# Kernel optimization log

Measured on AMD Instinct MI355X. Metric: run time of the kernel, lower is better.

Reference implementation:

```python
import jax, jax.numpy as jnp
import numpy as np

N_NODES = 100000


def _sage_conv(x, edge_index, W_n, W_s, b):
    # edge_index: [2, E] with row0 = src, row1 = dst (messages flow src -> dst)
    src, dst = edge_index[0], edge_index[1]
    msgs = x[src]                                   # [E, F] gather
    summed = jax.ops.segment_sum(msgs, dst, num_segments=N_NODES)   # [N, F]
    deg = jax.ops.segment_sum(jnp.ones((edge_index.shape[1],), x.dtype), dst,
                              num_segments=N_NODES)                 # [N]
    mean = summed / jnp.maximum(deg, 1.0)[:, None]  # mean aggregation
    return mean @ W_n + x @ W_s + b


def setup_inputs() -> dict:
    key = jax.random.key(0)
    ks = jax.random.split(key, 8)
    in_dim, hid_dim, out_dim = 64, 64, 32
    n_edges = 1600000
    x = jax.random.normal(ks[0], (N_NODES, in_dim), dtype=jnp.float32)
    edge_index = jax.random.randint(ks[1], (2, n_edges), 0, N_NODES, dtype=jnp.int64)
    s1 = 1.0 / np.sqrt(in_dim)
    s2 = 1.0 / np.sqrt(hid_dim)
    W1_n = jax.random.uniform(ks[2], (in_dim, hid_dim), jnp.float32, -s1, s1)
    W1_s = jax.random.uniform(ks[3], (in_dim, hid_dim), jnp.float32, -s1, s1)
    b1 = jnp.zeros((hid_dim,), jnp.float32)
    W2_n = jax.random.uniform(ks[4], (hid_dim, out_dim), jnp.float32, -s2, s2)
    W2_s = jax.random.uniform(ks[5], (hid_dim, out_dim), jnp.float32, -s2, s2)
    b2 = jnp.zeros((out_dim,), jnp.float32)
    return {"x": x, "edge_index": edge_index, "W1_n": W1_n, "W1_s": W1_s,
            "b1": b1, "W2_n": W2_n, "W2_s": W2_s, "b2": b2}


def reference(x, edge_index, W1_n, W1_s, b1, W2_n, W2_s, b2):
    h = _sage_conv(x, edge_index, W1_n, W1_s, b1)
    h = jax.nn.relu(h)
    # dropout(p=0.5) is identity in eval mode
    out = _sage_conv(h, edge_index, W2_n, W2_s, b2)
    return out
```

## Files before the change

### kernel.cpp

```cpp
#include <hip/hip_runtime.h>
#include <hip/hip_bf16.h>

#define N_NODES 100000
#define NB 784
#define NPAD 100352
#define BSH 7
#define BMASK 127
#define CAP 4096
#define APAD 68

__device__ inline void fma4(float a, const float4& w, float4& c) {
  c.x = fmaf(a, w.x, c.x);
  c.y = fmaf(a, w.y, c.y);
  c.z = fmaf(a, w.z, c.z);
  c.w = fmaf(a, w.w, c.w);
}
__device__ inline unsigned short f2bf(float f) {
  unsigned u = __float_as_uint(f);
  u += 0x7fffu + ((u >> 16) & 1u);
  return (unsigned short)(u >> 16);
}
__device__ inline float bflo(unsigned u) { return __uint_as_float(u << 16); }
__device__ inline float bfhi(unsigned u) { return __uint_as_float(u & 0xffff0000u); }

__global__ __launch_bounds__(256) void bscatter_k(const int* __restrict__ src,
                                                  const int* __restrict__ dst,
                                                  unsigned* __restrict__ bcur,
                                                  unsigned* __restrict__ ep,
                                                  int E) {
  __shared__ unsigned lh[NB];
  __shared__ unsigned lbase[NB];
  for (int i = threadIdx.x; i < NB; i += 256) lh[i] = 0;
  __syncthreads();
  const int base = blockIdx.x * 4096;
  unsigned short rank[16];
  unsigned short bb[16];
#pragma unroll
  for (int it = 0; it < 16; ++it) {
    int e = base + it * 256 + threadIdx.x;
    if (e < E) {
      unsigned b = ((unsigned)dst[e]) >> BSH;
      bb[it] = (unsigned short)b;
      rank[it] = (unsigned short)atomicAdd(&lh[b], 1u);
    }
  }
  __syncthreads();
  for (int i = threadIdx.x; i < NB; i += 256)
    lbase[i] = lh[i] ? atomicAdd(&bcur[i], lh[i]) : 0u;
  __syncthreads();
#pragma unroll
  for (int it = 0; it < 16; ++it) {
    int e = base + it * 256 + threadIdx.x;
    if (e < E) {
      unsigned b = bb[it];
      ep[(size_t)b * CAP + lbase[b] + rank[it]] =
          (((unsigned)src[e]) << BSH) | (((unsigned)dst[e]) & BMASK);
    }
  }
}

#define GB1 1563

__global__ __launch_bounds__(256) void fused1_k(
    const float* __restrict__ x, const float* __restrict__ W1n,
    const float* __restrict__ W1s, const float* __restrict__ b1,
    unsigned short* __restrict__ xnb, float* __restrict__ xs,
    const unsigned* __restrict__ ep, const unsigned* __restrict__ bcur,
    int* __restrict__ ssrc, uint2* __restrict__ rows2, int M) {
  __shared__ __align__(16) float smem[12544];
  const int tid = threadIdx.x;

  if (blockIdx.x >= GB1) {
    const int b = blockIdx.x - GB1;
    unsigned* cnt = (unsigned*)smem;
    unsigned* sc = cnt + 128;
    const unsigned cntb = bcur[b];
    const unsigned beg = (unsigned)(b * CAP);
    if (tid < 128) cnt[tid] = 0;
    __syncthreads();
    for (unsigned j = tid; j < cntb; j += 256)
      atomicAdd(&cnt[ep[(size_t)beg + j] & BMASK], 1u);
    __syncthreads();
    unsigned v = (tid < 128) ? cnt[tid] : 0u;
    if (tid < 128) sc[tid] = v;
    __syncthreads();
    for (int off = 1; off < 128; off <<= 1) {
      unsigned t = (tid < 128 && tid >= off) ? sc[tid - off] : 0u;
      __syncthreads();
      if (tid < 128) sc[tid] += t;
      __syncthreads();
    }
    if (tid < 128) {
      unsigned ex = sc[tid] - v;
      rows2[b * 128 + tid] = make_uint2(beg + ex, beg + ex + v);
      cnt[tid] = ex;
    }
    __syncthreads();
    for (unsigned j = tid; j < cntb; j += 256) {
      unsigned p = ep[(size_t)beg + j];
      unsigned r = atomicAdd(&cnt[p & BMASK], 1u);
      ssrc[(size_t)beg + r] = (int)(p >> BSH);
    }
    return;
  }

  float* Wn = smem;
  float* Ws = smem + 4096;
  float* Ax = smem + 8192;
  const int row0 = blockIdx.x * 64;

  for (int i = tid; i < 1024; i += 256) {
    ((float4*)Wn)[i] = ((const float4*)W1n)[i];
    ((float4*)Ws)[i] = ((const float4*)W1s)[i];
  }
  for (int i = tid; i < 1024; i += 256) {
    int r = i >> 4, c = i & 15;
    long long gr = row0 + r;
    if (gr >= M) gr = M - 1;
    float4 v = ((const float4*)(x + gr * 64))[c];
    *(float4*)&Ax[r * APAD + 4 * c] = v;
  }
  __syncthreads();

  const int tx = tid & 15;
  const int ty = tid >> 4;
  const int arow = ty * 4;

  float4 an[4], as[4];
#pragma unroll
  for (int r = 0; r < 4; ++r) {
    an[r] = make_float4(0.f, 0.f, 0.f, 0.f);
    as[r] = make_float4(0.f, 0.f, 0.f, 0.f);
  }

#pragma unroll 1
  for (int k4 = 0; k4 < 16; ++k4) {
    float4 wn0 = *(const float4*)&Wn[(4 * k4 + 0) * 64 + 4 * tx];
    float4 wn1 = *(const float4*)&Wn[(4 * k4 + 1) * 64 + 4 * tx];
    float4 wn2 = *(const float4*)&Wn[(4 * k4 + 2) * 64 + 4 * tx];
    float4 wn3 = *(const float4*)&Wn[(4 * k4 + 3) * 64 + 4 * tx];
    float4 ws0 = *(const float4*)&Ws[(4 * k4 + 0) * 64 + 4 * tx];
    float4 ws1 = *(const float4*)&Ws[(4 * k4 + 1) * 64 + 4 * tx];
    float4 ws2 = *(const float4*)&Ws[(4 * k4 + 2) * 64 + 4 * tx];
    float4 ws3 = *(const float4*)&Ws[(4 * k4 + 3) * 64 + 4 * tx];
#pragma unroll
    for (int r = 0; r < 4; ++r) {
      float4 a = *(const float4*)&Ax[(arow + r) * APAD + 4 * k4];
      fma4(a.x, wn0, an[r]);
      fma4(a.y, wn1, an[r]);
      fma4(a.z, wn2, an[r]);
      fma4(a.w, wn3, an[r]);
      fma4(a.x, ws0, as[r]);
      fma4(a.y, ws1, as[r]);
      fma4(a.z, ws2, as[r]);
      fma4(a.w, ws3, as[r]);
    }
  }

  const float4 bv = *(const float4*)&b1[4 * tx];
#pragma unroll
  for (int r = 0; r < 4; ++r) {
    int row = row0 + arow + r;
    if (row < M) {
      float4 o;
      o.x = as[r].x + bv.x;
      o.y = as[r].y + bv.y;
      o.z = as[r].z + bv.z;
      o.w = as[r].w + bv.w;
      *(float4*)&xs[(long long)row * 64 + 4 * tx] = o;
      ushort4 p;
      p.x = f2bf(an[r].x);
      p.y = f2bf(an[r].y);
      p.z = f2bf(an[r].z);
      p.w = f2bf(an[r].w);
      *(ushort4*)&xnb[(long long)row * 64 + 4 * tx] = p;
    }
  }
}

__global__ __launch_bounds__(256) void gemm2_k(
    const float* __restrict__ h, const float* __restrict__ W2n,
    const float* __restrict__ W2s, const float* __restrict__ b2,
    unsigned short* __restrict__ hnb, float* __restrict__ hs, int M) {
  __shared__ float Wn[64 * 32];
  __shared__ float Ws[64 * 32];
  __shared__ float Ah[128 * APAD];
  const int tid = threadIdx.x;
  const int row0 = blockIdx.x * 128;

  for (int i = tid; i < 512; i += 256) {
    ((float4*)Wn)[i] = ((const float4*)W2n)[i];
    ((float4*)Ws)[i] = ((const float4*)W2s)[i];
  }
  for (int i = tid; i < 2048; i += 256) {
    int r = i >> 4, c = i & 15;
    long long gr = row0 + r;
    if (gr >= M) gr = M - 1;
    float4 v = ((const float4*)(h + gr * 64))[c];
    *(float4*)&Ah[r * APAD + 4 * c] = v;
  }
  __syncthreads();

  const int tx = tid & 7;
  const int ty = tid >> 3;
  const int arow = ty * 4;

  float4 an[4], as[4];
#pragma unroll
  for (int r = 0; r < 4; ++r) {
    an[r] = make_float4(0.f, 0.f, 0.f, 0.f);
    as[r] = make_float4(0.f, 0.f, 0.f, 0.f);
  }

#pragma unroll 1
  for (int k4 = 0; k4 < 16; ++k4) {
    float4 wn0 = *(const float4*)&Wn[(4 * k4 + 0) * 32 + 4 * tx];
    float4 wn1 = *(const float4*)&Wn[(4 * k4 + 1) * 32 + 4 * tx];
    float4 wn2 = *(const float4*)&Wn[(4 * k4 + 2) * 32 + 4 * tx];
    float4 wn3 = *(const float4*)&Wn[(4 * k4 + 3) * 32 + 4 * tx];
    float4 ws0 = *(const float4*)&Ws[(4 * k4 + 0) * 32 + 4 * tx];
    float4 ws1 = *(const float4*)&Ws[(4 * k4 + 1) * 32 + 4 * tx];
    float4 ws2 = *(const float4*)&Ws[(4 * k4 + 2) * 32 + 4 * tx];
    float4 ws3 = *(const float4*)&Ws[(4 * k4 + 3) * 32 + 4 * tx];
#pragma unroll
    for (int r = 0; r < 4; ++r) {
      float4 a = *(const float4*)&Ah[(arow + r) * APAD + 4 * k4];
      fma4(a.x, wn0, an[r]);
      fma4(a.y, wn1, an[r]);
      fma4(a.z, wn2, an[r]);
      fma4(a.w, wn3, an[r]);
      fma4(a.x, ws0, as[r]);
      fma4(a.y, ws1, as[r]);
      fma4(a.z, ws2, as[r]);
      fma4(a.w, ws3, as[r]);
    }
  }

  const float4 bv = *(const float4*)&b2[4 * tx];
#pragma unroll
  for (int r = 0; r < 4; ++r) {
    int row = row0 + arow + r;
    if (row < M) {
      float4 o;
      o.x = as[r].x + bv.x;
      o.y = as[r].y + bv.y;
      o.z = as[r].z + bv.z;
      o.w = as[r].w + bv.w;
      *(float4*)&hs[(long long)row * 32 + 4 * tx] = o;
      ushort4 p;
      p.x = f2bf(an[r].x);
      p.y = f2bf(an[r].y);
      p.z = f2bf(an[r].z);
      p.w = f2bf(an[r].w);
      *(ushort4*)&hnb[(long long)row * 32 + 4 * tx] = p;
    }
  }
}

template <int LOGF, bool RELU>
__global__ __launch_bounds__(256) void gatherb_k(
    const uint4* __restrict__ valb4, const int* __restrict__ ssrc,
    const uint2* __restrict__ rows2, const float* __restrict__ base,
    float* __restrict__ out, int N) {
  constexpr int P = (1 << LOGF) / 8;
  const int node = blockIdx.x * (256 / P) + threadIdx.x / P;
  const int p = threadIdx.x & (P - 1);
  if (node >= N) return;
  const uint2 be = rows2[node];
  const unsigned beg = be.x, end = be.y;

  float acc[8];
#pragma unroll
  for (int q = 0; q < 8; ++q) acc[q] = 0.f;

  unsigned j = beg;
  for (; j + 8 <= end; j += 8) {
    int sn[8];
#pragma unroll
    for (int i = 0; i < 8; ++i) sn[i] = ssrc[j + i];
    uint4 u[8];
#pragma unroll
    for (int i = 0; i < 8; ++i) u[i] = valb4[(size_t)sn[i] * P + p];
#pragma unroll
    for (int i = 0; i < 8; ++i) {
      acc[0] += bflo(u[i].x);
      acc[1] += bfhi(u[i].x);
      acc[2] += bflo(u[i].y);
      acc[3] += bfhi(u[i].y);
      acc[4] += bflo(u[i].z);
      acc[5] += bfhi(u[i].z);
      acc[6] += bflo(u[i].w);
      acc[7] += bfhi(u[i].w);
    }
  }
  if (j < end) {
    const unsigned last = end - 1;
    int sn[8];
#pragma unroll
    for (int i = 0; i < 8; ++i) {
      unsigned jj = j + i;
      sn[i] = ssrc[jj < last ? jj : last];
    }
    uint4 u[8];
#pragma unroll
    for (int i = 0; i < 8; ++i) u[i] = valb4[(size_t)sn[i] * P + p];
#pragma unroll
    for (int i = 0; i < 8; ++i) {
      bool ok = (j + i) < end;
      acc[0] += ok ? bflo(u[i].x) : 0.f;
      acc[1] += ok ? bfhi(u[i].x) : 0.f;
      acc[2] += ok ? bflo(u[i].y) : 0.f;
      acc[3] += ok ? bfhi(u[i].y) : 0.f;
      acc[4] += ok ? bflo(u[i].z) : 0.f;
      acc[5] += ok ? bfhi(u[i].z) : 0.f;
      acc[6] += ok ? bflo(u[i].w) : 0.f;
      acc[7] += ok ? bfhi(u[i].w) : 0.f;
    }
  }

  const unsigned dg = end - beg;
  const float inv = dg ? 1.f / (float)dg : 0.f;
  const size_t o = (size_t)node * (8 * P) + 8 * p;
  float4 b0 = *(const float4*)&base[o];
  float4 b1 = *(const float4*)&base[o + 4];
  float4 o0, o1;
  o0.x = acc[0] * inv + b0.x;
  o0.y = acc[1] * inv + b0.y;
  o0.z = acc[2] * inv + b0.z;
  o0.w = acc[3] * inv + b0.w;
  o1.x = acc[4] * inv + b1.x;
  o1.y = acc[5] * inv + b1.y;
  o1.z = acc[6] * inv + b1.z;
  o1.w = acc[7] * inv + b1.w;
  if (RELU) {
    o0.x = fmaxf(o0.x, 0.f);
    o0.y = fmaxf(o0.y, 0.f);
    o0.z = fmaxf(o0.z, 0.f);
    o0.w = fmaxf(o0.w, 0.f);
    o1.x = fmaxf(o1.x, 0.f);
    o1.y = fmaxf(o1.y, 0.f);
    o1.z = fmaxf(o1.z, 0.f);
    o1.w = fmaxf(o1.w, 0.f);
  }
  *(float4*)&out[o] = o0;
  *(float4*)&out[o + 4] = o1;
}

extern "C" void kernel_launch(void* const* d_in, const int* in_sizes, int n_in,
                              void* d_out, int out_size, void* d_ws,
                              size_t ws_size, hipStream_t stream) {
  const float* x   = (const float*)d_in[0];
  const int*   ei  = (const int*)d_in[1];
  const float* W1n = (const float*)d_in[2];
  const float* W1s = (const float*)d_in[3];
  const float* b1  = (const float*)d_in[4];
  const float* W2n = (const float*)d_in[5];
  const float* W2s = (const float*)d_in[6];
  const float* b2  = (const float*)d_in[7];
  float* out = (float*)d_out;

  const int E = in_sizes[1] / 2;
  const int M = N_NODES;
  const int* src = ei;
  const int* dst = ei + E;

  char* wsb = (char*)d_ws;
  unsigned*       ep    = (unsigned*)(wsb);
  int*            ssrc  = (int*)(wsb + 12845056);
  uint2*          rows2 = (uint2*)(wsb + 25690112);
  unsigned*       bcur  = (unsigned*)(wsb + 26492928);
  unsigned short* xnb   = (unsigned short*)(wsb + 26496064);
  float*          xs    = (float*)(wsb + 39296064);
  float*          h     = (float*)(wsb + 64896064);
  unsigned short* hnb   = xnb;
  float*          hs    = xs;

  hipMemsetAsync(bcur, 0, NB * 4, stream);
  bscatter_k<<<(E + 4095) / 4096, 256, 0, stream>>>(src, dst, bcur, ep, E);
  fused1_k<<<GB1 + NB, 256, 0, stream>>>(x, W1n, W1s, b1, xnb, xs, ep, bcur,
                                         ssrc, rows2, M);
  gatherb_k<6, true><<<(M + 31) / 32, 256, 0, stream>>>(
      (const uint4*)xnb, ssrc, rows2, xs, h, M);
  gemm2_k<<<(M + 127) / 128, 256, 0, stream>>>(h, W2n, W2s, b2, hnb, hs, M);
  gatherb_k<5, false><<<(M + 63) / 64, 256, 0, stream>>>(
      (const uint4*)hnb, ssrc, rows2, hs, out, M);
}
```

Baseline: 237.1 us.

## Store layer-1 mean as bf16 and fuse residual+ReLU into layer-2 GEMM load

The layer-1 gather now writes only the mean aggregation, packed as bf16. The self-term add and ReLU move into the gemm2 tile load, which reads both the bf16 mean and the fp32 self term. This halves the gather's write traffic and avoids reading the self term in the gather, but adds another bf16 rounding of the hidden activations before they reach the second layer. The bucket-scatter kernel also moves to 1024-thread blocks, each handling 16K edges, to cut global atomics. Workspace buffers are remapped so that hnb reuses the edge-pointer region and hs the former h region.

```diff
diff --git a/kernel.cpp b/kernel.cpp
--- a/kernel.cpp
+++ b/kernel.cpp
@@ -20,24 +20,30 @@
   u += 0x7fffu + ((u >> 16) & 1u);
   return (unsigned short)(u >> 16);
 }
+__device__ inline unsigned pack2bf(float a, float b) {
+  return (unsigned)f2bf(a) | ((unsigned)f2bf(b) << 16);
+}
 __device__ inline float bflo(unsigned u) { return __uint_as_float(u << 16); }
 __device__ inline float bfhi(unsigned u) { return __uint_as_float(u & 0xffff0000u); }
-
-__global__ __launch_bounds__(256) void bscatter_k(const int* __restrict__ src,
-                                                  const int* __restrict__ dst,
-                                                  unsigned* __restrict__ bcur,
-                                                  unsigned* __restrict__ ep,
-                                                  int E) {
+__device__ inline float bf2f(unsigned short u) {
+  return __uint_as_float((unsigned)u << 16);
+}
+
+__global__ __launch_bounds__(1024) void bscatter_k(const int* __restrict__ src,
+                                                   const int* __restrict__ dst,
+                                                   unsigned* __restrict__ bcur,
+                                                   unsigned* __restrict__ ep,
+                                                   int E) {
   __shared__ unsigned lh[NB];
   __shared__ unsigned lbase[NB];
-  for (int i = threadIdx.x; i < NB; i += 256) lh[i] = 0;
+  for (int i = threadIdx.x; i < NB; i += 1024) lh[i] = 0;
   __syncthreads();
-  const int base = blockIdx.x * 4096;
+  const int base = blockIdx.x * 16384;
   unsigned short rank[16];
   unsigned short bb[16];
 #pragma unroll
   for (int it = 0; it < 16; ++it) {
-    int e = base + it * 256 + threadIdx.x;
+    int e = base + it * 1024 + threadIdx.x;
     if (e < E) {
       unsigned b = ((unsigned)dst[e]) >> BSH;
       bb[it] = (unsigned short)b;
@@ -45,12 +51,12 @@
     }
   }
   __syncthreads();
-  for (int i = threadIdx.x; i < NB; i += 256)
+  for (int i = threadIdx.x; i < NB; i += 1024)
     lbase[i] = lh[i] ? atomicAdd(&bcur[i], lh[i]) : 0u;
   __syncthreads();
 #pragma unroll
   for (int it = 0; it < 16; ++it) {
-    int e = base + it * 256 + threadIdx.x;
+    int e = base + it * 1024 + threadIdx.x;
     if (e < E) {
       unsigned b = bb[it];
       ep[(size_t)b * CAP + lbase[b] + rank[it]] =
@@ -178,10 +184,80 @@
   }
 }
 
+__global__ __launch_bounds__(256) void gather1_k(
+    const uint4* __restrict__ valb4, const int* __restrict__ ssrc,
+    const uint2* __restrict__ rows2, uint4* __restrict__ meanb, int N) {
+  constexpr int P = 8;
+  const int node = blockIdx.x * (256 / P) + threadIdx.x / P;
+  const int p = threadIdx.x & (P - 1);
+  if (node >= N) return;
+  const uint2 be = rows2[node];
+  const unsigned beg = be.x, end = be.y;
+
+  float acc[8];
+#pragma unroll
+  for (int q = 0; q < 8; ++q) acc[q] = 0.f;
+
+  unsigned j = beg;
+  for (; j + 8 <= end; j += 8) {
+    int sn[8];
+#pragma unroll
+    for (int i = 0; i < 8; ++i) sn[i] = ssrc[j + i];
+    uint4 u[8];
+#pragma unroll
+    for (int i = 0; i < 8; ++i) u[i] = valb4[(size_t)sn[i] * P + p];
+#pragma unroll
+    for (int i = 0; i < 8; ++i) {
+      acc[0] += bflo(u[i].x);
+      acc[1] += bfhi(u[i].x);
+      acc[2] += bflo(u[i].y);
+      acc[3] += bfhi(u[i].y);
+      acc[4] += bflo(u[i].z);
+      acc[5] += bfhi(u[i].z);
+      acc[6] += bflo(u[i].w);
+      acc[7] += bfhi(u[i].w);
+    }
+  }
+  if (j < end) {
+    const unsigned last = end - 1;
+    int sn[8];
+#pragma unroll
+    for (int i = 0; i < 8; ++i) {
+      unsigned jj = j + i;
+      sn[i] = ssrc[jj < last ? jj : last];
+    }
+    uint4 u[8];
+#pragma unroll
+    for (int i = 0; i < 8; ++i) u[i] = valb4[(size_t)sn[i] * P + p];
+#pragma unroll
+    for (int i = 0; i < 8; ++i) {
+      bool ok = (j + i) < end;
+      acc[0] += ok ? bflo(u[i].x) : 0.f;
+      acc[1] += ok ? bfhi(u[i].x) : 0.f;
+      acc[2] += ok ? bflo(u[i].y) : 0.f;
+      acc[3] += ok ? bfhi(u[i].y) : 0.f;
+      acc[4] += ok ? bflo(u[i].z) : 0.f;
+      acc[5] += ok ? bfhi(u[i].z) : 0.f;
+      acc[6] += ok ? bflo(u[i].w) : 0.f;
+      acc[7] += ok ? bfhi(u[i].w) : 0.f;
+    }
+  }
+
+  const unsigned dg = end - beg;
+  const float inv = dg ? 1.f / (float)dg : 0.f;
+  uint4 pk;
+  pk.x = pack2bf(acc[0] * inv, acc[1] * inv);
+  pk.y = pack2bf(acc[2] * inv, acc[3] * inv);
+  pk.z = pack2bf(acc[4] * inv, acc[5] * inv);
+  pk.w = pack2bf(acc[6] * inv, acc[7] * inv);
+  meanb[(size_t)node * P + p] = pk;
+}
+
 __global__ __launch_bounds__(256) void gemm2_k(
-    const float* __restrict__ h, const float* __restrict__ W2n,
-    const float* __restrict__ W2s, const float* __restrict__ b2,
-    unsigned short* __restrict__ hnb, float* __restrict__ hs, int M) {
+    const unsigned short* __restrict__ mean1, const float* __restrict__ xs,
+    const float* __restrict__ W2n, const float* __restrict__ W2s,
+    const float* __restrict__ b2, unsigned short* __restrict__ hnb,
+    float* __restrict__ hs, int M) {
   __shared__ float Wn[64 * 32];
   __shared__ float Ws[64 * 32];
   __shared__ float Ah[128 * APAD];
@@ -196,7 +272,13 @@
     int r = i >> 4, c = i & 15;
     long long gr = row0 + r;
     if (gr >= M) gr = M - 1;
-    float4 v = ((const float4*)(h + gr * 64))[c];
+    float4 sv = ((const float4*)(xs + gr * 64))[c];
+    ushort4 mv = ((const ushort4*)(mean1 + gr * 64))[c];
+    float4 v;
+    v.x = fmaxf(bf2f(mv.x) + sv.x, 0.f);
+    v.y = fmaxf(bf2f(mv.y) + sv.y, 0.f);
+    v.z = fmaxf(bf2f(mv.z) + sv.z, 0.f);
+    v.w = fmaxf(bf2f(mv.w) + sv.w, 0.f);
     *(float4*)&Ah[r * APAD + 4 * c] = v;
   }
   __syncthreads();
@@ -257,12 +339,11 @@
   }
 }
 
-template <int LOGF, bool RELU>
-__global__ __launch_bounds__(256) void gatherb_k(
+__global__ __launch_bounds__(256) void gather2_k(
     const uint4* __restrict__ valb4, const int* __restrict__ ssrc,
     const uint2* __restrict__ rows2, const float* __restrict__ base,
     float* __restrict__ out, int N) {
-  constexpr int P = (1 << LOGF) / 8;
+  constexpr int P = 4;
   const int node = blockIdx.x * (256 / P) + threadIdx.x / P;
   const int p = threadIdx.x & (P - 1);
   if (node >= N) return;
@@ -320,7 +401,7 @@
 
   const unsigned dg = end - beg;
   const float inv = dg ? 1.f / (float)dg : 0.f;
-  const size_t o = (size_t)node * (8 * P) + 8 * p;
+  const size_t o = (size_t)node * 32 + 8 * p;
   float4 b0 = *(const float4*)&base[o];
   float4 b1 = *(const float4*)&base[o + 4];
   float4 o0, o1;
@@ -332,16 +413,6 @@
   o1.y = acc[5] * inv + b1.y;
   o1.z = acc[6] * inv + b1.z;
   o1.w = acc[7] * inv + b1.w;
-  if (RELU) {
-    o0.x = fmaxf(o0.x, 0.f);
-    o0.y = fmaxf(o0.y, 0.f);
-    o0.z = fmaxf(o0.z, 0.f);
-    o0.w = fmaxf(o0.w, 0.f);
-    o1.x = fmaxf(o1.x, 0.f);
-    o1.y = fmaxf(o1.y, 0.f);
-    o1.z = fmaxf(o1.z, 0.f);
-    o1.w = fmaxf(o1.w, 0.f);
-  }
   *(float4*)&out[o] = o0;
   *(float4*)&out[o + 4] = o1;
 }
@@ -371,17 +442,18 @@
   unsigned*       bcur  = (unsigned*)(wsb + 26492928);
   unsigned short* xnb   = (unsigned short*)(wsb + 26496064);
   float*          xs    = (float*)(wsb + 39296064);
-  float*          h     = (float*)(wsb + 64896064);
-  unsigned short* hnb   = xnb;
-  float*          hs    = xs;
+  unsigned short* mean1 = (unsigned short*)(wsb + 64896064);
+  unsigned short* hnb   = (unsigned short*)(wsb);
+  float*          hs    = (float*)(wsb + 64896064);
 
   hipMemsetAsync(bcur, 0, NB * 4, stream);
-  bscatter_k<<<(E + 4095) / 4096, 256, 0, stream>>>(src, dst, bcur, ep, E);
+  bscatter_k<<<(E + 16383) / 16384, 1024, 0, stream>>>(src, dst, bcur, ep, E);
   fused1_k<<<GB1 + NB, 256, 0, stream>>>(x, W1n, W1s, b1, xnb, xs, ep, bcur,
                                          ssrc, rows2, M);
-  gatherb_k<6, true><<<(M + 31) / 32, 256, 0, stream>>>(
-      (const uint4*)xnb, ssrc, rows2, xs, h, M);
-  gemm2_k<<<(M + 127) / 128, 256, 0, stream>>>(h, W2n, W2s, b2, hnb, hs, M);
-  gatherb_k<5, false><<<(M + 63) / 64, 256, 0, stream>>>(
-      (const uint4*)hnb, ssrc, rows2, hs, out, M);
-}
+  gather1_k<<<(M + 31) / 32, 256, 0, stream>>>((const uint4*)xnb, ssrc, rows2,
+                                               (uint4*)mean1, M);
+  gemm2_k<<<(M + 127) / 128, 256, 0, stream>>>(mean1, xs, W2n, W2s, b2, hnb,
+                                               hs, M);
+  gather2_k<<<(M + 63) / 64, 256, 0, stream>>>((const uint4*)hnb, ssrc, rows2,
+                                               hs, out, M);
+}
```

After: 236.4 us. No clear change (-0.3%).
